# Optimization experiments

Measured on AMD Instinct MI355X. Metric: run time of the kernel, lower is better.

Reference implementation:

```python
import jax, jax.numpy as jnp
import numpy as np

RADIUS = 4
SIGMA_1 = 5.0
SIGMA_2 = 1.0


def _gaussian_kernel(dtype):
    # norm.pdf(d)/norm.pdf(0) == exp(-d^2/2)
    x2 = jnp.linspace(-RADIUS, RADIUS, 2 * RADIUS + 1) ** 2
    dist = jnp.sqrt(x2[:, None] + x2[None, :]) / SIGMA_1
    return jnp.exp(-0.5 * dist ** 2).astype(dtype)  # [k, k]


def setup_inputs() -> dict:
    key = jax.random.key(0)
    k1, k2 = jax.random.split(key)
    labels = jax.random.uniform(k1, (16, 20, 256, 256), dtype=jnp.float32)
    inputs = jax.random.uniform(k2, (16, 3, 256, 256), dtype=jnp.float32)
    return {"labels": labels, "inputs": inputs}


def reference(labels, inputs):
    B, K, H, W = labels.shape
    kernel = _gaussian_kernel(labels.dtype)

    # per-class mean color: mean(inputs * probs, HW) / (mean(probs, HW) + 1e-5)
    pmean = jnp.mean(labels, axis=(2, 3))                           # [B, K]
    xmean = jnp.einsum('bchw,bkhw->bkc', inputs, labels) / (H * W)  # [B, K, C]
    class_mean = xmean / (pmean[..., None] + 1e-5)                  # [B, K, C]

    # diff = sum_c (x_c - m_c)^2, expanded to avoid a [B,K,C,H,W] intermediate
    x2sum = jnp.sum(inputs ** 2, axis=1)                            # [B, H, W]
    cross = jnp.einsum('bchw,bkc->bkhw', inputs, class_mean)        # [B, K, H, W]
    m2 = jnp.sum(class_mean ** 2, axis=-1)                          # [B, K]
    diff = x2sum[:, None] - 2.0 * cross + m2[:, :, None, None]      # [B, K, H, W]
    weights = jnp.exp(-(diff ** 2) / (SIGMA_2 ** 2))                # [B, K, H, W]

    def blur(x):  # single-channel gaussian conv, vectorized over B*K
        lhs = x.reshape(B * K, 1, H, W)
        rhs = kernel[None, None]  # [1, 1, k, k]
        y = jax.lax.conv_general_dilated(
            lhs, rhs, window_strides=(1, 1),
            padding=[(RADIUS, RADIUS), (RADIUS, RADIUS)],
            dimension_numbers=('NCHW', 'OIHW', 'NCHW'))
        return y.reshape(B, K, H, W)

    num = jnp.sum(labels * blur(labels * weights), axis=(0, 2, 3))  # [K]
    den = jnp.sum(labels * blur(weights), axis=(0, 2, 3))           # [K]
    loss = jnp.sum(jnp.abs(num / (den + 1e-6)))
    return jnp.asarray(K, labels.dtype) - loss
```

## Files before the change

### kernel.cpp

```cpp
#include <hip/hip_runtime.h>

#define B_ 16
#define K_ 20
#define H_ 256
#define W_ 256
#define HW_ (H_*W_)
#define BK_ (B_*K_)
#define TH_ 16
#define KT_ 5
#define SCH_ 16
#define NBLK_FUSED_ (4*K_*B_)

#define WS_ND_   (SCH_*4*BK_)
#define WS_CNT_  (WS_ND_ + 2*NBLK_FUSED_)

#define G1T 0.980198673f
#define G2T 0.923116346f
#define G3T 0.835270211f
#define G4T 0.726149037f

__device__ __forceinline__ float4 zero4() { return make_float4(0.f, 0.f, 0.f, 0.f); }
__device__ __forceinline__ float rfl(float v) {
    return __int_as_float(__builtin_amdgcn_readfirstlane(__float_as_int(v)));
}

__global__ __launch_bounds__(256) void stats_k(const float* __restrict__ labels,
                                               const float* __restrict__ inputs,
                                               float* __restrict__ ws) {
    const int x = threadIdx.x;
    const int chunk = blockIdx.x;
    const int kt = blockIdx.y;
    const int b  = blockIdx.z;
    const int k0 = kt * KT_;
    if (chunk == 0 && kt == 0 && b == 0 && x == 0)
        ((unsigned*)(ws + WS_CNT_))[0] = 0u;

    const int cbase = chunk * (16 * W_ / 4);
    const float4* in0 = (const float4*)inputs + (size_t)b * 3 * (HW_/4) + cbase;
    const float4* in1 = in0 + (HW_/4);
    const float4* in2 = in1 + (HW_/4);
    const float4* lb  = (const float4*)labels + (size_t)(b * K_ + k0) * (HW_/4) + cbase;

    float acc[KT_][4];
#pragma unroll
    for (int kk = 0; kk < KT_; ++kk)
        acc[kk][0] = acc[kk][1] = acc[kk][2] = acc[kk][3] = 0.f;

#pragma unroll
    for (int it = 0; it < 4; ++it) {
        const int idx = it * 256 + x;
        const float4 a0 = in0[idx];
        const float4 a1 = in1[idx];
        const float4 a2 = in2[idx];
        float4 lv[KT_];
#pragma unroll
        for (int kk = 0; kk < KT_; ++kk) lv[kk] = lb[kk * (HW_/4) + idx];
#pragma unroll
        for (int kk = 0; kk < KT_; ++kk) {
            const float4 l = lv[kk];
            acc[kk][0] += (l.x + l.y) + (l.z + l.w);
            acc[kk][1] += fmaf(l.w, a0.w, fmaf(l.z, a0.z, fmaf(l.y, a0.y, l.x * a0.x)));
            acc[kk][2] += fmaf(l.w, a1.w, fmaf(l.z, a1.z, fmaf(l.y, a1.y, l.x * a1.x)));
            acc[kk][3] += fmaf(l.w, a2.w, fmaf(l.z, a2.z, fmaf(l.y, a2.y, l.x * a2.x)));
        }
    }

#pragma unroll
    for (int kk = 0; kk < KT_; ++kk)
#pragma unroll
        for (int q = 0; q < 4; ++q)
            for (int o = 32; o > 0; o >>= 1)
                acc[kk][q] += __shfl_down(acc[kk][q], o);

    __shared__ float sred[4][KT_][4];
    const int widx = x >> 6, lane = x & 63;
    if (lane == 0)
#pragma unroll
        for (int kk = 0; kk < KT_; ++kk)
#pragma unroll
            for (int q = 0; q < 4; ++q) sred[widx][kk][q] = acc[kk][q];
    __syncthreads();
    if (x < KT_ * 4) {
        const int kk = x >> 2, q = x & 3;
        const float v = sred[0][kk][q] + sred[1][kk][q] + sred[2][kk][q] + sred[3][kk][q];
        ws[(chunk * 4 + q) * BK_ + b * K_ + k0 + kk] = v;
    }
}

__device__ __forceinline__ void hblur4(const float4 v, const int lane, float o[4]) {
    float u0 = __shfl_up(v.x, 1), u1 = __shfl_up(v.y, 1);
    float u2 = __shfl_up(v.z, 1), u3 = __shfl_up(v.w, 1);
    float d0 = __shfl_down(v.x, 1), d1 = __shfl_down(v.y, 1);
    float d2 = __shfl_down(v.z, 1), d3 = __shfl_down(v.w, 1);
    if (lane == 0)  { u0 = u1 = u2 = u3 = 0.f; }
    if (lane == 63) { d0 = d1 = d2 = d3 = 0.f; }
    o[0] = fmaf(G4T, u0 + d0, fmaf(G3T, u1 + v.w, fmaf(G2T, u2 + v.z, fmaf(G1T, u3 + v.y, v.x))));
    o[1] = fmaf(G4T, u1 + d1, fmaf(G3T, u2 + d0,  fmaf(G2T, u3 + v.w, fmaf(G1T, v.x + v.z, v.y))));
    o[2] = fmaf(G4T, u2 + d2, fmaf(G3T, u3 + d1,  fmaf(G2T, v.x + d0, fmaf(G1T, v.y + v.w, v.z))));
    o[3] = fmaf(G4T, u3 + d3, fmaf(G3T, v.x + d2, fmaf(G2T, v.y + d1, fmaf(G1T, v.z + d0,  v.w))));
}

__global__ __launch_bounds__(256) void fused_k(const float* __restrict__ labels,
                                               const float* __restrict__ inputs,
                                               float* __restrict__ ws,
                                               float* __restrict__ out) {
    const int x = threadIdx.x;
    const int lane = x & 63;
    const int widx = x >> 6;
    const int bid = blockIdx.x;
    const int swz = (bid & 7) * (NBLK_FUSED_ / 8) + (bid >> 3);
    const int b   = swz / (4 * K_);
    const int rem = swz - b * (4 * K_);
    const int k   = rem >> 2;
    const int sg  = rem & 3;
    const int bk  = b * K_ + k;
    const int r0  = (sg * 4 + widx) * TH_;

    float s0 = 0.f, s1 = 0.f, s2 = 0.f, s3 = 0.f;
#pragma unroll
    for (int c = 0; c < SCH_; ++c) {
        const float* p = ws + c * 4 * BK_;
        s0 += p[bk]; s1 += p[BK_ + bk]; s2 += p[2*BK_ + bk]; s3 += p[3*BK_ + bk];
    }
    const float dnv = s0 + 1e-5f * (float)HW_;
    const float c0 = s1 / dnv, c1 = s2 / dnv, c2 = s3 / dnv;
    const float tc0 = rfl(2.f * c0), tc1 = rfl(2.f * c1), tc2 = rfl(2.f * c2);
    const float m2v = rfl(c0*c0 + c1*c1 + c2*c2);

    const float4* lb4  = (const float4*)labels + (size_t)bk * (HW_/4);
    const float4* in04 = (const float4*)inputs + (size_t)b * 3 * (HW_/4);
    const float4* in14 = in04 + (HW_/4);
    const float4* in24 = in14 + (HW_/4);

    float rhl[8][4];
#pragma unroll
    for (int i = 0; i < 8; ++i) {
        const int gr = r0 - 4 + i;
        float4 l = zero4();
        if ((unsigned)gr < (unsigned)H_) l = lb4[gr * (W_/4) + lane];
        hblur4(l, lane, rhl[i]);
    }

    float4 hl = lb4[(r0 + 4) * (W_/4) + lane];
    float4 h0 = in04[r0 * (W_/4) + lane];
    float4 h1 = in14[r0 * (W_/4) + lane];
    float4 h2 = in24[r0 * (W_/4) + lane];

    float num = 0.f, den = 0.f;
#pragma unroll 1
    for (int ro = 0; ro < TH_ / 8; ++ro) {
#pragma unroll
        for (int u = 0; u < 8; ++u) {
            const int orow = r0 + ro * 8 + u;
            float4 nl = zero4();
            if (orow + 5 < H_) nl = lb4[(orow + 5) * (W_/4) + lane];
            const int nir = (orow + 1 < H_) ? orow + 1 : H_ - 1;
            const float4 n0 = in04[nir * (W_/4) + lane];
            const float4 n1 = in14[nir * (W_/4) + lane];
            const float4 n2 = in24[nir * (W_/4) + lane];
            const float4 lo4 = lb4[orow * (W_/4) + lane];
            const int s0i = u, s1i = (u+1)&7, s2i = (u+2)&7, s3i = (u+3)&7;
            const int s4i = (u+4)&7, s5i = (u+5)&7, s6i = (u+6)&7, s7i = (u+7)&7;
            float part[4];
#pragma unroll
            for (int c = 0; c < 4; ++c)
                part[c] = fmaf(G3T, rhl[s1i][c] + rhl[s7i][c],
                          fmaf(G2T, rhl[s2i][c] + rhl[s6i][c],
                          fmaf(G1T, rhl[s3i][c] + rhl[s5i][c], rhl[s4i][c])));
            const float d0 = fmaf(h0.x, h0.x - tc0, fmaf(h1.x, h1.x - tc1, fmaf(h2.x, h2.x - tc2, m2v)));
            const float d1 = fmaf(h0.y, h0.y - tc0, fmaf(h1.y, h1.y - tc1, fmaf(h2.y, h2.y - tc2, m2v)));
            const float d2 = fmaf(h0.z, h0.z - tc0, fmaf(h1.z, h1.z - tc1, fmaf(h2.z, h2.z - tc2, m2v)));
            const float d3 = fmaf(h0.w, h0.w - tc0, fmaf(h1.w, h1.w - tc1, fmaf(h2.w, h2.w - tc2, m2v)));
            const float wv[4] = {__expf(-d0*d0), __expf(-d1*d1), __expf(-d2*d2), __expf(-d3*d3)};
            float cur[4];
            hblur4(hl, lane, cur);
            const float loa[4] = {lo4.x, lo4.y, lo4.z, lo4.w};
#pragma unroll
            for (int c = 0; c < 4; ++c) {
                const float bl = fmaf(G4T, rhl[s0i][c] + cur[c], part[c]);
                const float t  = wv[c] * bl;
                den += t;
                num = fmaf(loa[c], t, num);
            }
#pragma unroll
            for (int c = 0; c < 4; ++c) rhl[u][c] = cur[c];
            hl = nl; h0 = n0; h1 = n1; h2 = n2;
        }
    }

    for (int o = 32; o > 0; o >>= 1) { num += __shfl_down(num, o); den += __shfl_down(den, o); }
    __shared__ float rb[4][2];
    __shared__ unsigned sdone;
    if (lane == 0) { rb[widx][0] = num; rb[widx][1] = den; }
    __syncthreads();
    if (x == 0) {
        const float fn = rb[0][0] + rb[1][0] + rb[2][0] + rb[3][0];
        const float fd = rb[0][1] + rb[1][1] + rb[2][1] + rb[3][1];
        float2* nd2 = (float2*)(ws + WS_ND_);
        nd2[k * 64 + b * 4 + sg] = make_float2(fn, fd);
        __threadfence();
        sdone = atomicAdd((unsigned*)(ws + WS_CNT_), 1u);
    }
    __syncthreads();
    if (sdone == (unsigned)(NBLK_FUSED_ - 1)) {
        __threadfence();
        if (x < 64) {
            float term = 0.f;
            if (x < K_) {
                const float2* nd2 = (const float2*)(ws + WS_ND_);
                float ns = 0.f, ds = 0.f;
                for (int i = 0; i < 64; ++i) {
                    const float2 v = nd2[x * 64 + i];
                    ns += v.x; ds += v.y;
                }
                term = fabsf(ns / (ds + 1e-6f));
            }
            for (int o = 32; o > 0; o >>= 1) term += __shfl_down(term, o);
            if (x == 0) out[0] = (float)K_ - term;
        }
    }
}

extern "C" void kernel_launch(void* const* d_in, const int* in_sizes, int n_in,
                              void* d_out, int out_size, void* d_ws, size_t ws_size,
                              hipStream_t stream) {
    const float* labels = (const float*)d_in[0];
    const float* inputs = (const float*)d_in[1];
    float* ws = (float*)d_ws;

    stats_k<<<dim3(SCH_, K_ / KT_, B_), 256, 0, stream>>>(labels, inputs, ws);
    fused_k<<<NBLK_FUSED_, 256, 0, stream>>>(labels, inputs, ws, (float*)d_out);
}
```

Before: 208.0 us.

## Restructure blur to column-per-thread with 64-row tiles and LDS horizontal pass

Each block now covers a 64-row strip with one column per thread, instead of each wave covering 16 rows with float4 per lane. The vertical blur runs from a register ring buffer and the horizontal blur runs through a double-buffered shared-memory row. The goal is to cut the halo-row label reloads and replace the cross-lane shuffles. In exchange it adds a block-wide barrier per row, uses scalar instead of vector loads, and gives each thread less instruction-level parallelism.

```diff
diff --git a/kernel.cpp b/kernel.cpp
--- a/kernel.cpp
+++ b/kernel.cpp
@@ -6,7 +6,7 @@
 #define W_ 256
 #define HW_ (H_*W_)
 #define BK_ (B_*K_)
-#define TH_ 16
+#define TH_ 64
 #define KT_ 5
 #define SCH_ 16
 #define NBLK_FUSED_ (4*K_*B_)
@@ -19,7 +19,6 @@
 #define G3T 0.835270211f
 #define G4T 0.726149037f
 
-__device__ __forceinline__ float4 zero4() { return make_float4(0.f, 0.f, 0.f, 0.f); }
 __device__ __forceinline__ float rfl(float v) {
     return __int_as_float(__builtin_amdgcn_readfirstlane(__float_as_int(v)));
 }
@@ -87,26 +86,11 @@
     }
 }
 
-__device__ __forceinline__ void hblur4(const float4 v, const int lane, float o[4]) {
-    float u0 = __shfl_up(v.x, 1), u1 = __shfl_up(v.y, 1);
-    float u2 = __shfl_up(v.z, 1), u3 = __shfl_up(v.w, 1);
-    float d0 = __shfl_down(v.x, 1), d1 = __shfl_down(v.y, 1);
-    float d2 = __shfl_down(v.z, 1), d3 = __shfl_down(v.w, 1);
-    if (lane == 0)  { u0 = u1 = u2 = u3 = 0.f; }
-    if (lane == 63) { d0 = d1 = d2 = d3 = 0.f; }
-    o[0] = fmaf(G4T, u0 + d0, fmaf(G3T, u1 + v.w, fmaf(G2T, u2 + v.z, fmaf(G1T, u3 + v.y, v.x))));
-    o[1] = fmaf(G4T, u1 + d1, fmaf(G3T, u2 + d0,  fmaf(G2T, u3 + v.w, fmaf(G1T, v.x + v.z, v.y))));
-    o[2] = fmaf(G4T, u2 + d2, fmaf(G3T, u3 + d1,  fmaf(G2T, v.x + d0, fmaf(G1T, v.y + v.w, v.z))));
-    o[3] = fmaf(G4T, u3 + d3, fmaf(G3T, v.x + d2, fmaf(G2T, v.y + d1, fmaf(G1T, v.z + d0,  v.w))));
-}
-
 __global__ __launch_bounds__(256) void fused_k(const float* __restrict__ labels,
                                                const float* __restrict__ inputs,
                                                float* __restrict__ ws,
                                                float* __restrict__ out) {
     const int x = threadIdx.x;
-    const int lane = x & 63;
-    const int widx = x >> 6;
     const int bid = blockIdx.x;
     const int swz = (bid & 7) * (NBLK_FUSED_ / 8) + (bid >> 3);
     const int b   = swz / (4 * K_);
@@ -114,7 +98,7 @@
     const int k   = rem >> 2;
     const int sg  = rem & 3;
     const int bk  = b * K_ + k;
-    const int r0  = (sg * 4 + widx) * TH_;
+    const int r0  = sg * TH_;
 
     float s0 = 0.f, s1 = 0.f, s2 = 0.f, s3 = 0.f;
 #pragma unroll
@@ -127,24 +111,29 @@
     const float tc0 = rfl(2.f * c0), tc1 = rfl(2.f * c1), tc2 = rfl(2.f * c2);
     const float m2v = rfl(c0*c0 + c1*c1 + c2*c2);
 
-    const float4* lb4  = (const float4*)labels + (size_t)bk * (HW_/4);
-    const float4* in04 = (const float4*)inputs + (size_t)b * 3 * (HW_/4);
-    const float4* in14 = in04 + (HW_/4);
-    const float4* in24 = in14 + (HW_/4);
-
-    float rhl[8][4];
+    const float* lb  = labels + (size_t)bk * HW_;
+    const float* i0p = inputs + (size_t)b * 3 * HW_;
+    const float* i1p = i0p + HW_;
+    const float* i2p = i1p + HW_;
+
+    __shared__ float sv[2][W_ + 8];
+    if (x < 4) {
+        sv[0][x] = 0.f; sv[0][W_ + 4 + x] = 0.f;
+        sv[1][x] = 0.f; sv[1][W_ + 4 + x] = 0.f;
+    }
+
+    float rl[8];
 #pragma unroll
     for (int i = 0; i < 8; ++i) {
         const int gr = r0 - 4 + i;
-        float4 l = zero4();
-        if ((unsigned)gr < (unsigned)H_) l = lb4[gr * (W_/4) + lane];
-        hblur4(l, lane, rhl[i]);
-    }
-
-    float4 hl = lb4[(r0 + 4) * (W_/4) + lane];
-    float4 h0 = in04[r0 * (W_/4) + lane];
-    float4 h1 = in14[r0 * (W_/4) + lane];
-    float4 h2 = in24[r0 * (W_/4) + lane];
+        rl[i] = (gr >= 0) ? lb[gr * W_ + x] : 0.f;
+    }
+    float hl  = lb[(r0 + 4) * W_ + x];
+    float hi0 = i0p[r0 * W_ + x];
+    float hi1 = i1p[r0 * W_ + x];
+    float hi2 = i2p[r0 * W_ + x];
+
+    __syncthreads();
 
     float num = 0.f, den = 0.f;
 #pragma unroll 1
@@ -152,45 +141,41 @@
 #pragma unroll
         for (int u = 0; u < 8; ++u) {
             const int orow = r0 + ro * 8 + u;
-            float4 nl = zero4();
-            if (orow + 5 < H_) nl = lb4[(orow + 5) * (W_/4) + lane];
+            float nl = 0.f;
+            if (orow + 5 < H_) nl = lb[(orow + 5) * W_ + x];
             const int nir = (orow + 1 < H_) ? orow + 1 : H_ - 1;
-            const float4 n0 = in04[nir * (W_/4) + lane];
-            const float4 n1 = in14[nir * (W_/4) + lane];
-            const float4 n2 = in24[nir * (W_/4) + lane];
-            const float4 lo4 = lb4[orow * (W_/4) + lane];
-            const int s0i = u, s1i = (u+1)&7, s2i = (u+2)&7, s3i = (u+3)&7;
-            const int s4i = (u+4)&7, s5i = (u+5)&7, s6i = (u+6)&7, s7i = (u+7)&7;
-            float part[4];
-#pragma unroll
-            for (int c = 0; c < 4; ++c)
-                part[c] = fmaf(G3T, rhl[s1i][c] + rhl[s7i][c],
-                          fmaf(G2T, rhl[s2i][c] + rhl[s6i][c],
-                          fmaf(G1T, rhl[s3i][c] + rhl[s5i][c], rhl[s4i][c])));
-            const float d0 = fmaf(h0.x, h0.x - tc0, fmaf(h1.x, h1.x - tc1, fmaf(h2.x, h2.x - tc2, m2v)));
-            const float d1 = fmaf(h0.y, h0.y - tc0, fmaf(h1.y, h1.y - tc1, fmaf(h2.y, h2.y - tc2, m2v)));
-            const float d2 = fmaf(h0.z, h0.z - tc0, fmaf(h1.z, h1.z - tc1, fmaf(h2.z, h2.z - tc2, m2v)));
-            const float d3 = fmaf(h0.w, h0.w - tc0, fmaf(h1.w, h1.w - tc1, fmaf(h2.w, h2.w - tc2, m2v)));
-            const float wv[4] = {__expf(-d0*d0), __expf(-d1*d1), __expf(-d2*d2), __expf(-d3*d3)};
-            float cur[4];
-            hblur4(hl, lane, cur);
-            const float loa[4] = {lo4.x, lo4.y, lo4.z, lo4.w};
-#pragma unroll
-            for (int c = 0; c < 4; ++c) {
-                const float bl = fmaf(G4T, rhl[s0i][c] + cur[c], part[c]);
-                const float t  = wv[c] * bl;
-                den += t;
-                num = fmaf(loa[c], t, num);
-            }
-#pragma unroll
-            for (int c = 0; c < 4; ++c) rhl[u][c] = cur[c];
-            hl = nl; h0 = n0; h1 = n1; h2 = n2;
+            const float ni0 = i0p[nir * W_ + x];
+            const float ni1 = i1p[nir * W_ + x];
+            const float ni2 = i2p[nir * W_ + x];
+            const float vbl = fmaf(G4T, rl[u] + hl,
+                              fmaf(G3T, rl[(u+1)&7] + rl[(u+7)&7],
+                              fmaf(G2T, rl[(u+2)&7] + rl[(u+6)&7],
+                              fmaf(G1T, rl[(u+3)&7] + rl[(u+5)&7], rl[(u+4)&7]))));
+            const int bf = u & 1;
+            sv[bf][4 + x] = vbl;
+            __syncthreads();
+            const float* s = &sv[bf][x];
+            const float bl = fmaf(G4T, s[0] + s[8],
+                             fmaf(G3T, s[1] + s[7],
+                             fmaf(G2T, s[2] + s[6],
+                             fmaf(G1T, s[3] + s[5], s[4]))));
+            const float d = fmaf(hi0, hi0 - tc0,
+                            fmaf(hi1, hi1 - tc1,
+                            fmaf(hi2, hi2 - tc2, m2v)));
+            const float w = __expf(-d * d);
+            const float t = w * bl;
+            den += t;
+            num = fmaf(rl[(u + 4) & 7], t, num);
+            rl[u] = hl;
+            hl = nl; hi0 = ni0; hi1 = ni1; hi2 = ni2;
         }
     }
 
+    const int widx = x >> 6, lane = x & 63;
     for (int o = 32; o > 0; o >>= 1) { num += __shfl_down(num, o); den += __shfl_down(den, o); }
     __shared__ float rb[4][2];
     __shared__ unsigned sdone;
+    __syncthreads();
     if (lane == 0) { rb[widx][0] = num; rb[widx][1] = den; }
     __syncthreads();
     if (x == 0) {
```

Result: faster. 197.6 us (-5.0%).
